# Optimization experiments

Hardware: AMD Instinct MI355X
Metric: run time of the kernel (lower is better)

## Reference

```python
import jax, jax.numpy as jnp
import numpy as np

D_MODEL = 512
N_HEADS = 8
D_HEAD = 64
D_FF = 1024
EPS = 1e-5


def setup_inputs() -> dict:
    key = jax.random.key(0)
    ks = jax.random.split(key, 9)
    B, L = 4, 2048
    s = lambda fan_in: 1.0 / np.sqrt(fan_in)
    return {
        "x": jax.random.normal(ks[0], (B, L, D_MODEL), dtype=jnp.float32),
        "ln1_w": jnp.ones((D_MODEL,), jnp.float32),
        "ln1_b": jnp.zeros((D_MODEL,), jnp.float32),
        "ln2_w": jnp.ones((D_MODEL,), jnp.float32),
        "ln2_b": jnp.zeros((D_MODEL,), jnp.float32),
        "wq": jax.random.normal(ks[1], (D_MODEL, N_HEADS * D_HEAD), jnp.float32) * s(D_MODEL),
        "wk": jax.random.normal(ks[2], (D_MODEL, N_HEADS * D_HEAD), jnp.float32) * s(D_MODEL),
        "wv": jax.random.normal(ks[3], (D_MODEL, N_HEADS * D_HEAD), jnp.float32) * s(D_MODEL),
        "wo": jax.random.normal(ks[4], (N_HEADS * D_HEAD, D_MODEL), jnp.float32) * s(N_HEADS * D_HEAD),
        "w_gate": jax.random.normal(ks[5], (D_MODEL, D_FF), jnp.float32) * s(D_MODEL),
        "w_up": jax.random.normal(ks[6], (D_MODEL, D_FF), jnp.float32) * s(D_MODEL),
        "w_down": jax.random.normal(ks[7], (D_FF, D_MODEL), jnp.float32) * s(D_FF),
    }


def _layernorm(x, w, b):
    mu = jnp.mean(x, axis=-1, keepdims=True)
    var = jnp.var(x, axis=-1, keepdims=True)
    return (x - mu) * jax.lax.rsqrt(var + EPS) * w + b


def reference(x, ln1_w, ln1_b, ln2_w, ln2_b, wq, wk, wv, wo, w_gate, w_up, w_down):
    B, L, _ = x.shape
    scale = D_HEAD ** -0.5

    # --- attention sublayer (pre-LN residual) ---
    h = _layernorm(x, ln1_w, ln1_b)
    q = (h @ wq).reshape(B, L, N_HEADS, D_HEAD)  # [B,L,H,Dh]
    k = (h @ wk).reshape(B, L, N_HEADS, D_HEAD)
    v = (h @ wv).reshape(B, L, N_HEADS, D_HEAD)
    scores = jnp.einsum("bqhd,bkhd->bhqk", q, k) * scale
    # softmax computed in fp32, cast back (matches F.softmax(dtype=float32).to(q.dtype))
    attn = jax.nn.softmax(scores.astype(jnp.float32), axis=-1).astype(q.dtype)
    out = jnp.einsum("bhqk,bkhd->bqhd", attn, v).reshape(B, L, N_HEADS * D_HEAD)
    x = x + out @ wo

    # --- SwiGLU FFN sublayer (pre-LN residual) ---
    h = _layernorm(x, ln2_w, ln2_b)
    gate = jax.nn.silu(h @ w_gate)
    x = x + (gate * (h @ w_up)) @ w_down
    return x
```

## Files before the change

### kernel.cpp

```cpp
#include <hip/hip_runtime.h>
#include <hip/hip_bf16.h>
#include <math.h>

#define EPS 1e-5f

typedef __attribute__((ext_vector_type(8))) short bf16x8;
typedef __attribute__((ext_vector_type(4))) float f32x4;

__device__ __forceinline__ short f2bf(float x) {
    union { float f; unsigned u; } un; un.f = x;
    unsigned r = un.u + 0x7FFF + ((un.u >> 16) & 1);
    return (short)(r >> 16);
}
__device__ __forceinline__ float bf2f(short s) {
    union { unsigned u; float f; } un;
    un.u = ((unsigned)(unsigned short)s) << 16;
    return un.f;
}
__device__ __forceinline__ unsigned pack_bf2(float a, float b) {
    unsigned r;
    asm("v_cvt_pk_bf16_f32 %0, %1, %2" : "=v"(r) : "v"(a), "v"(b));
    return r;
}
__device__ __forceinline__ float exp2_fast(float x) {
    float r;
    asm("v_exp_f32 %0, %1" : "=v"(r) : "v"(x));
    return r;
}
__device__ __forceinline__ void load_lds16(const short* g, short* l) {
    __builtin_amdgcn_global_load_lds(
        (const __attribute__((address_space(1))) unsigned int*)g,
        (__attribute__((address_space(3))) unsigned int*)l, 16, 0, 0);
}

__global__ __launch_bounds__(256) void ln_kernel_b(const float* __restrict__ in,
                                                   const float* __restrict__ w,
                                                   const float* __restrict__ bb,
                                                   short* __restrict__ out) {
    int row = blockIdx.x;
    const float* x = in + (size_t)row * 512;
    short* o = out + (size_t)row * 512;
    int t = threadIdx.x;
    float v0 = x[t], v1 = x[t + 256];
    float s = v0 + v1;
    float s2 = v0 * v0 + v1 * v1;
    for (int off = 32; off > 0; off >>= 1) {
        s  += __shfl_down(s, off);
        s2 += __shfl_down(s2, off);
    }
    __shared__ float rs_[4], rs2_[4];
    __shared__ float mu_s, rstd_s;
    int wid = t >> 6;
    if ((t & 63) == 0) { rs_[wid] = s; rs2_[wid] = s2; }
    __syncthreads();
    if (t == 0) {
        float ts  = rs_[0] + rs_[1] + rs_[2] + rs_[3];
        float ts2 = rs2_[0] + rs2_[1] + rs2_[2] + rs2_[3];
        float mu  = ts * (1.f / 512.f);
        float var = ts2 * (1.f / 512.f) - mu * mu;
        mu_s = mu;
        rstd_s = rsqrtf(var + EPS);
    }
    __syncthreads();
    float mu = mu_s, rstd = rstd_s;
    o[t]       = f2bf((v0 - mu) * rstd * w[t]       + bb[t]);
    o[t + 256] = f2bf((v1 - mu) * rstd * w[t + 256] + bb[t + 256]);
}

struct WT { const float* w; short* t; int K; int N; };
struct WT7 { WT a[7]; };
__global__ __launch_bounds__(256) void transp_w_kernel(WT7 p) {
    WT e = p.a[blockIdx.z];
    int k0 = blockIdx.x * 32, n0 = blockIdx.y * 32;
    if (k0 >= e.K || n0 >= e.N) return;
    __shared__ short t[32][33];
    int tx = threadIdx.x & 31, ty = threadIdx.x >> 5;
#pragma unroll
    for (int pp = 0; pp < 4; pp++)
        t[pp * 8 + ty][tx] = f2bf(e.w[(size_t)(k0 + pp * 8 + ty) * e.N + n0 + tx]);
    __syncthreads();
#pragma unroll
    for (int pp = 0; pp < 4; pp++)
        e.t[(size_t)(n0 + pp * 8 + ty) * e.K + k0 + tx] = t[tx][pp * 8 + ty];
}

template <int EPI>
__global__ __launch_bounds__(256) void gemm_mfma(const short* __restrict__ A,
                                                 const short* __restrict__ Bt,
                                                 const float* __restrict__ res,
                                                 void* __restrict__ Cv,
                                                 int M, int N, int K) {
    __shared__ short As[128 * 64];
    __shared__ short Bs[128 * 64];
    const int tid = threadIdx.x;
    const int lane = tid & 63, w = tid >> 6;
    const int g = lane >> 4, r16 = lane & 15;
    const int wr = w >> 1, wc = w & 1;

    const int nb = gridDim.x * gridDim.y;
    const int fid = blockIdx.y * gridDim.x + blockIdx.x;
    const int nid = (fid & 7) * (nb >> 3) + (fid >> 3);
    const int m0 = (nid / gridDim.x) * 128, n0 = (nid % gridDim.x) * 128;

    const int lr = lane >> 3;
    const int ck = (lane & 7) ^ lr;
    const int row0 = w * 32;

    f32x4 acc[4][4] = {};

    for (int k0 = 0; k0 < K; k0 += 64) {
        __syncthreads();
#pragma unroll
        for (int p = 0; p < 4; p++) {
            int rb = row0 + p * 8;
            load_lds16(&A [(size_t)(m0 + rb + lr) * K + k0 + ck * 8], &As[rb * 64]);
            load_lds16(&Bt[(size_t)(n0 + rb + lr) * K + k0 + ck * 8], &Bs[rb * 64]);
        }
        __syncthreads();
#pragma unroll
        for (int ks = 0; ks < 2; ks++) {
            bf16x8 av[4], bv[4];
#pragma unroll
            for (int i = 0; i < 4; i++) {
                int row = wr * 64 + i * 16 + r16;
                av[i] = *(const bf16x8*)&As[row * 64 + ((ks * 4 + g) ^ (row & 7)) * 8];
            }
#pragma unroll
            for (int j = 0; j < 4; j++) {
                int row = wc * 64 + j * 16 + r16;
                bv[j] = *(const bf16x8*)&Bs[row * 64 + ((ks * 4 + g) ^ (row & 7)) * 8];
            }
#pragma unroll
            for (int i = 0; i < 4; i++)
#pragma unroll
                for (int j = 0; j < 4; j++)
                    acc[i][j] = __builtin_amdgcn_mfma_f32_16x16x32_bf16(av[i], bv[j], acc[i][j], 0, 0, 0);
        }
    }

#pragma unroll
    for (int i = 0; i < 4; i++)
#pragma unroll
        for (int j = 0; j < 4; j++)
#pragma unroll
            for (int jr = 0; jr < 4; jr++) {
                int m = m0 + wr * 64 + i * 16 + 4 * g + jr;
                int n = n0 + wc * 64 + j * 16 + r16;
                float v = acc[i][j][jr];
                if (EPI == 0) {
                    size_t idx = (size_t)m * N + n;
                    ((float*)Cv)[idx] = res[idx] + v;
                } else if (EPI == 2) {
                    if (n < 512) v *= 0.18033688011112042f;
                    ((short*)Cv)[(size_t)(n >> 9) * 4194304 +
                                 (((size_t)(m >> 11) * 8 + ((n >> 6) & 7)) * 2048 + (m & 2047)) * 64 + (n & 63)] = f2bf(v);
                } else {
                    ((short*)Cv)[(size_t)(n >> 10) * 8388608 + (size_t)m * 1024 + (n & 1023)] = f2bf(v);
                }
            }
}

__global__ __launch_bounds__(256) void transp_v_kernel(const short* __restrict__ vb,
                                                       short* __restrict__ vt) {
    __shared__ short tile[64][65];
    int l0 = blockIdx.x * 64;
    int bh = blockIdx.y;
    const size_t base = (size_t)bh * 2048 * 64;
    int tid = threadIdx.x;
#pragma unroll
    for (int p = 0; p < 4; p++) {
        int r = p * 16 + (tid >> 4);
        int c4 = (tid & 15) * 4;
        *(short4*)&tile[r][c4] = *(const short4*)&vb[base + (size_t)(l0 + r) * 64 + c4];
    }
    __syncthreads();
#pragma unroll
    for (int p = 0; p < 4; p++) {
        int d = p * 16 + (tid >> 4);
        int c4 = (tid & 15) * 4;
        short4 o;
        o.x = tile[c4 + 0][d]; o.y = tile[c4 + 1][d];
        o.z = tile[c4 + 2][d]; o.w = tile[c4 + 3][d];
        *(short4*)&vt[base + (size_t)d * 2048 + l0 + c4] = o;
    }
}

__global__ __launch_bounds__(256) void attn_mfma_kernel(const short* __restrict__ qb,
                                                        const short* __restrict__ kb,
                                                        const short* __restrict__ vt,
                                                        short* __restrict__ outb) {
    __shared__ short QP[4096];
    __shared__ short Ks[2][4096];
    __shared__ short Vs[2][4096];

    const int fid = blockIdx.y * 32 + blockIdx.x;
    const int nid = (fid & 7) * 128 + (fid >> 3);
    const int bh = nid >> 5, qt = nid & 31;
    const int b = bh >> 3, h = bh & 7;
    const int q0 = qt * 64;
    const size_t hb = (size_t)bh * (2048 * 64);

    const int tid = threadIdx.x;
    const int lane = tid & 63, w = tid >> 6;
    const int g = lane >> 4, r16 = lane & 15;
    const int lr = lane >> 3, ck = (lane & 7) ^ lr;
    const int rx = r16 & 7;

    load_lds16(&qb[hb + (size_t)(q0 + 16 * w + lr) * 64 + ck * 8], &QP[(16 * w) * 64]);
    load_lds16(&qb[hb + (size_t)(q0 + 16 * w + 8 + lr) * 64 + ck * 8], &QP[(16 * w + 8) * 64]);

    auto stageKV = [&](int buf, int kt) {
        int k0 = kt * 64;
        int rb = w * 16;
        load_lds16(&kb[hb + (size_t)(k0 + rb + lr) * 64 + ck * 8],      &Ks[buf][rb * 64]);
        load_lds16(&kb[hb + (size_t)(k0 + rb + 8 + lr) * 64 + ck * 8],  &Ks[buf][(rb + 8) * 64]);
        load_lds16(&vt[hb + (size_t)(rb + lr) * 2048 + k0 + ck * 8],     &Vs[buf][rb * 64]);
        load_lds16(&vt[hb + (size_t)(rb + 8 + lr) * 2048 + k0 + ck * 8], &Vs[buf][(rb + 8) * 64]);
    };
    stageKV(0, 0);

    bf16x8 aq0, aq1;
    float m_ = -1e30f, l_ = 0.f;
    f32x4 ot[4] = {};
    int cur = 0;

    for (int t = 0; t < 32; t++) {
        __syncthreads();
        if (t == 0) {
            int row = 16 * w + r16;
            aq0 = *(const bf16x8*)&QP[row * 64 + ((0 + g) ^ rx) * 8];
            aq1 = *(const bf16x8*)&QP[row * 64 + ((4 + g) ^ rx) * 8];
        }
        if (t + 1 < 32) stageKV(cur ^ 1, t + 1);
        const short* Kc = &Ks[cur][0];
        const short* Vc = &Vs[cur][0];

        f32x4 s[4];
#pragma unroll
        for (int c = 0; c < 4; c++) {
            int row = 16 * c + r16;
            bf16x8 ak0 = *(const bf16x8*)&Kc[row * 64 + ((0 + g) ^ rx) * 8];
            bf16x8 ak1 = *(const bf16x8*)&Kc[row * 64 + ((4 + g) ^ rx) * 8];
            f32x4 acc = {};
            acc = __builtin_amdgcn_mfma_f32_16x16x32_bf16(ak0, aq0, acc, 0, 0, 0);
            acc = __builtin_amdgcn_mfma_f32_16x16x32_bf16(ak1, aq1, acc, 0, 0, 0);
            s[c] = acc;
        }

        float pmax = s[0][0];
#pragma unroll
        for (int c = 0; c < 4; c++)
#pragma unroll
            for (int jr = 0; jr < 4; jr++)
                if (c || jr) pmax = fmaxf(pmax, s[c][jr]);
        pmax = fmaxf(pmax, __shfl_xor(pmax, 16));
        pmax = fmaxf(pmax, __shfl_xor(pmax, 32));
        if (!__all(pmax - m_ <= 8.f)) {
            float mn = fmaxf(m_, pmax);
            float al = exp2_fast(m_ - mn);
            l_ *= al;
#pragma unroll
            for (int c = 0; c < 4; c++) ot[c] *= al;
            m_ = mn;
        }
        float rs = 0.f;
#pragma unroll
        for (int c = 0; c < 4; c++) {
            float p0 = exp2_fast(s[c][0] - m_);
            float p1 = exp2_fast(s[c][1] - m_);
            float p2 = exp2_fast(s[c][2] - m_);
            float p3 = exp2_fast(s[c][3] - m_);
            rs += (p0 + p1) + (p2 + p3);
            unsigned lo = pack_bf2(p0, p1);
            unsigned hi = pack_bf2(p2, p3);
            int colbase = 16 * c + 4 * g;
            int si = (16 * w + r16) * 64 + (((colbase >> 3) ^ rx) * 8) + (colbase & 7);
            *(unsigned*)&QP[si] = lo;
            *(unsigned*)&QP[si + 2] = hi;
        }
        rs += __shfl_xor(rs, 16);
        rs += __shfl_xor(rs, 32);
        l_ += rs;

        int prow = 16 * w + r16;
        bf16x8 bp0 = *(const bf16x8*)&QP[prow * 64 + ((0 + g) ^ rx) * 8];
        bf16x8 bp1 = *(const bf16x8*)&QP[prow * 64 + ((4 + g) ^ rx) * 8];
#pragma unroll
        for (int c = 0; c < 4; c++) {
            int row = 16 * c + r16;
            bf16x8 av0 = *(const bf16x8*)&Vc[row * 64 + ((0 + g) ^ rx) * 8];
            bf16x8 av1 = *(const bf16x8*)&Vc[row * 64 + ((4 + g) ^ rx) * 8];
            ot[c] = __builtin_amdgcn_mfma_f32_16x16x32_bf16(av0, bp0, ot[c], 0, 0, 0);
            ot[c] = __builtin_amdgcn_mfma_f32_16x16x32_bf16(av1, bp1, ot[c], 0, 0, 0);
        }
        cur ^= 1;
    }

    float inv = 1.f / l_;
    int q = q0 + 16 * w + r16;
#pragma unroll
    for (int c = 0; c < 4; c++) {
        unsigned lo = pack_bf2(ot[c][0] * inv, ot[c][1] * inv);
        unsigned hi = pack_bf2(ot[c][2] * inv, ot[c][3] * inv);
        int d = 16 * c + 4 * g;
        size_t oi = ((size_t)b * 2048 + q) * 512 + h * 64 + d;
        *(unsigned*)&outb[oi] = lo;
        *(unsigned*)&outb[oi + 2] = hi;
    }
}

__global__ __launch_bounds__(256) void silumul_b_kernel(const short* __restrict__ g,
                                                        const short* __restrict__ u,
                                                        short* __restrict__ o) {
    size_t i = ((size_t)blockIdx.x * 256 + threadIdx.x) * 8;
    bf16x8 gv = *(const bf16x8*)&g[i];
    bf16x8 uv = *(const bf16x8*)&u[i];
    bf16x8 ov;
#pragma unroll
    for (int j = 0; j < 8; j++) {
        float x = bf2f(gv[j]);
        float y = x / (1.f + __expf(-x)) * bf2f(uv[j]);
        ov[j] = f2bf(y);
    }
    *(bf16x8*)&o[i] = ov;
}

extern "C" void kernel_launch(void* const* d_in, const int* in_sizes, int n_in,
                              void* d_out, int out_size, void* d_ws, size_t ws_size,
                              hipStream_t stream) {
    const float* x      = (const float*)d_in[0];
    const float* ln1_w  = (const float*)d_in[1];
    const float* ln1_b  = (const float*)d_in[2];
    const float* ln2_w  = (const float*)d_in[3];
    const float* ln2_b  = (const float*)d_in[4];
    const float* wq     = (const float*)d_in[5];
    const float* wk     = (const float*)d_in[6];
    const float* wv     = (const float*)d_in[7];
    const float* wo     = (const float*)d_in[8];
    const float* w_gate = (const float*)d_in[9];
    const float* w_up   = (const float*)d_in[10];
    const float* w_down = (const float*)d_in[11];
    float* out = (float*)d_out;

    const int M = 4 * 2048;
    char* ws = (char*)d_ws;
    const size_t MB = 1 << 20;
    short* h1b   = (short*)(ws);
    short* qb    = (short*)(ws + 8 * MB);
    short* kb    = (short*)(ws + 16 * MB);
    short* vb    = (short*)(ws + 24 * MB);
    short* vt    = (short*)(ws + 32 * MB);
    short* aob   = (short*)(ws + 40 * MB);
    short* g_b   = (short*)(ws + 48 * MB);
    short* u_b   = (short*)(ws + 64 * MB);
    short* qkvT  = (short*)(ws + 80 * MB);
    short* woT   = (short*)(ws + 82 * MB);
    short* wguT  = (short*)(ws + 83 * MB);
    short* wdT   = (short*)(ws + 85 * MB);
    short* h2b   = qb;

    WT7 wt;
    wt.a[0] = {wq,     qkvT,               512,  512};
    wt.a[1] = {wk,     qkvT + 512 * 512,   512,  512};
    wt.a[2] = {wv,     qkvT + 1024 * 512,  512,  512};
    wt.a[3] = {wo,     woT,                512,  512};
    wt.a[4] = {w_gate, wguT,               512, 1024};
    wt.a[5] = {w_up,   wguT + 1024 * 512,  512, 1024};
    wt.a[6] = {w_down, wdT,               1024,  512};

    transp_w_kernel<<<dim3(32, 32, 7), 256, 0, stream>>>(wt);
    ln_kernel_b<<<M, 256, 0, stream>>>(x, ln1_w, ln1_b, h1b);
    gemm_mfma<2><<<dim3(12, 64), 256, 0, stream>>>(h1b, qkvT, nullptr, qb, M, 1536, 512);
    transp_v_kernel<<<dim3(32, 32), 256, 0, stream>>>(vb, vt);
    attn_mfma_kernel<<<dim3(32, 32), 256, 0, stream>>>(qb, kb, vt, aob);
    gemm_mfma<0><<<dim3(4, 64), 256, 0, stream>>>(aob, woT, x, out, M, 512, 512);
    ln_kernel_b<<<M, 256, 0, stream>>>(out, ln2_w, ln2_b, h2b);
    gemm_mfma<3><<<dim3(16, 64), 256, 0, stream>>>(h2b, wguT, nullptr, g_b, M, 2048, 512);
    silumul_b_kernel<<<(M * 1024 / 8 + 255) / 256, 256, 0, stream>>>(g_b, u_b, g_b);
    gemm_mfma<0><<<dim3(4, 64), 256, 0, stream>>>(g_b, wdT, out, out, M, 512, 1024);
}
```

Baseline: 192.1 us.

## Widen attention query tile, fuse SiLU-mul into up GEMM, vectorize layernorm

Three changes. The attention kernel now handles 128 queries per block (two 16-row groups per wave), so each staged K/V tile is reused for twice as many queries and the grid is halved. The gate/up GEMM is split in two, and the up GEMM's epilogue reads the gate output and applies SiLU times up directly, which removes the separate elementwise kernel. LayerNorm now runs one row per wave with float4 loads and a shuffle-only reduction, with no shared memory or block barriers. The trade-offs are higher register pressure in attention, fewer attention blocks for occupancy, and an extra gate-tensor read in the GEMM epilogue.

Result: faster. 183.1 us (-4.7%).

```diff
diff --git a/kernel.cpp b/kernel.cpp
--- a/kernel.cpp
+++ b/kernel.cpp
@@ -37,34 +37,31 @@
                                                    const float* __restrict__ w,
                                                    const float* __restrict__ bb,
                                                    short* __restrict__ out) {
-    int row = blockIdx.x;
-    const float* x = in + (size_t)row * 512;
-    short* o = out + (size_t)row * 512;
-    int t = threadIdx.x;
-    float v0 = x[t], v1 = x[t + 256];
-    float s = v0 + v1;
-    float s2 = v0 * v0 + v1 * v1;
-    for (int off = 32; off > 0; off >>= 1) {
-        s  += __shfl_down(s, off);
-        s2 += __shfl_down(s2, off);
-    }
-    __shared__ float rs_[4], rs2_[4];
-    __shared__ float mu_s, rstd_s;
-    int wid = t >> 6;
-    if ((t & 63) == 0) { rs_[wid] = s; rs2_[wid] = s2; }
-    __syncthreads();
-    if (t == 0) {
-        float ts  = rs_[0] + rs_[1] + rs_[2] + rs_[3];
-        float ts2 = rs2_[0] + rs2_[1] + rs2_[2] + rs2_[3];
-        float mu  = ts * (1.f / 512.f);
-        float var = ts2 * (1.f / 512.f) - mu * mu;
-        mu_s = mu;
-        rstd_s = rsqrtf(var + EPS);
-    }
-    __syncthreads();
-    float mu = mu_s, rstd = rstd_s;
-    o[t]       = f2bf((v0 - mu) * rstd * w[t]       + bb[t]);
-    o[t + 256] = f2bf((v1 - mu) * rstd * w[t + 256] + bb[t + 256]);
+    int wv = threadIdx.x >> 6, lane = threadIdx.x & 63;
+    int row = blockIdx.x * 4 + wv;
+    const float* x = in + (size_t)row * 512 + lane * 8;
+    float4 v0 = *(const float4*)x;
+    float4 v1 = *(const float4*)(x + 4);
+    float s  = (v0.x + v0.y) + (v0.z + v0.w) + (v1.x + v1.y) + (v1.z + v1.w);
+    float s2 = v0.x*v0.x + v0.y*v0.y + v0.z*v0.z + v0.w*v0.w
+             + v1.x*v1.x + v1.y*v1.y + v1.z*v1.z + v1.w*v1.w;
+#pragma unroll
+    for (int off = 1; off < 64; off <<= 1) {
+        s  += __shfl_xor(s, off);
+        s2 += __shfl_xor(s2, off);
+    }
+    float mu = s * (1.f / 512.f);
+    float rstd = rsqrtf(s2 * (1.f / 512.f) - mu * mu + EPS);
+    const float4 wa = *(const float4*)&w[lane * 8];
+    const float4 wb = *(const float4*)&w[lane * 8 + 4];
+    const float4 ba = *(const float4*)&bb[lane * 8];
+    const float4 bv = *(const float4*)&bb[lane * 8 + 4];
+    uint4 o;
+    o.x = pack_bf2((v0.x - mu) * rstd * wa.x + ba.x, (v0.y - mu) * rstd * wa.y + ba.y);
+    o.y = pack_bf2((v0.z - mu) * rstd * wa.z + ba.z, (v0.w - mu) * rstd * wa.w + ba.w);
+    o.z = pack_bf2((v1.x - mu) * rstd * wb.x + bv.x, (v1.y - mu) * rstd * wb.y + bv.y);
+    o.w = pack_bf2((v1.z - mu) * rstd * wb.z + bv.z, (v1.w - mu) * rstd * wb.w + bv.w);
+    *(uint4*)&out[(size_t)row * 512 + lane * 8] = o;
 }
 
 struct WT { const float* w; short* t; int K; int N; };
@@ -88,6 +85,7 @@
 __global__ __launch_bounds__(256) void gemm_mfma(const short* __restrict__ A,
                                                  const short* __restrict__ Bt,
                                                  const float* __restrict__ res,
+                                                 const short* __restrict__ resb,
                                                  void* __restrict__ Cv,
                                                  int M, int N, int K) {
     __shared__ short As[128 * 64];
@@ -150,12 +148,16 @@
                 if (EPI == 0) {
                     size_t idx = (size_t)m * N + n;
                     ((float*)Cv)[idx] = res[idx] + v;
+                } else if (EPI == 1) {
+                    ((short*)Cv)[(size_t)m * N + n] = f2bf(v);
                 } else if (EPI == 2) {
                     if (n < 512) v *= 0.18033688011112042f;
                     ((short*)Cv)[(size_t)(n >> 9) * 4194304 +
                                  (((size_t)(m >> 11) * 8 + ((n >> 6) & 7)) * 2048 + (m & 2047)) * 64 + (n & 63)] = f2bf(v);
                 } else {
-                    ((short*)Cv)[(size_t)(n >> 10) * 8388608 + (size_t)m * 1024 + (n & 1023)] = f2bf(v);
+                    float gt = bf2f(resb[(size_t)m * N + n]);
+                    float y = gt / (1.f + __expf(-gt)) * v;
+                    ((short*)Cv)[(size_t)m * N + n] = f2bf(y);
                 }
             }
 }
@@ -189,15 +191,15 @@
                                                         const short* __restrict__ kb,
                                                         const short* __restrict__ vt,
                                                         short* __restrict__ outb) {
-    __shared__ short QP[4096];
+    __shared__ short QP[128 * 64];
     __shared__ short Ks[2][4096];
     __shared__ short Vs[2][4096];
 
-    const int fid = blockIdx.y * 32 + blockIdx.x;
-    const int nid = (fid & 7) * 128 + (fid >> 3);
-    const int bh = nid >> 5, qt = nid & 31;
+    const int fid = blockIdx.y * gridDim.x + blockIdx.x;
+    const int nid = (fid & 7) * 64 + (fid >> 3);
+    const int bh = nid >> 4, qt = nid & 15;
     const int b = bh >> 3, h = bh & 7;
-    const int q0 = qt * 64;
+    const int q0 = qt * 128;
     const size_t hb = (size_t)bh * (2048 * 64);
 
     const int tid = threadIdx.x;
@@ -206,8 +208,10 @@
     const int lr = lane >> 3, ck = (lane & 7) ^ lr;
     const int rx = r16 & 7;
 
-    load_lds16(&qb[hb + (size_t)(q0 + 16 * w + lr) * 64 + ck * 8], &QP[(16 * w) * 64]);
-    load_lds16(&qb[hb + (size_t)(q0 + 16 * w + 8 + lr) * 64 + ck * 8], &QP[(16 * w + 8) * 64]);
+#pragma unroll
+    for (int p = 0; p < 4; p++)
+        load_lds16(&qb[hb + (size_t)(q0 + 32 * w + 8 * p + lr) * 64 + ck * 8],
+                   &QP[(32 * w + 8 * p) * 64]);
 
     auto stageKV = [&](int buf, int kt) {
         int k0 = kt * 64;
@@ -219,110 +223,119 @@
     };
     stageKV(0, 0);
 
-    bf16x8 aq0, aq1;
-    float m_ = -1e30f, l_ = 0.f;
-    f32x4 ot[4] = {};
+    bf16x8 aqA0, aqA1, aqB0, aqB1;
+    float mA = -1e30f, lA = 0.f, mB = -1e30f, lB = 0.f;
+    f32x4 oA[4] = {}, oB[4] = {};
     int cur = 0;
 
     for (int t = 0; t < 32; t++) {
         __syncthreads();
         if (t == 0) {
-            int row = 16 * w + r16;
-            aq0 = *(const bf16x8*)&QP[row * 64 + ((0 + g) ^ rx) * 8];
-            aq1 = *(const bf16x8*)&QP[row * 64 + ((4 + g) ^ rx) * 8];
+            int rowA = 32 * w + r16, rowB = rowA + 16;
+            aqA0 = *(const bf16x8*)&QP[rowA * 64 + ((0 + g) ^ rx) * 8];
+            aqA1 = *(const bf16x8*)&QP[rowA * 64 + ((4 + g) ^ rx) * 8];
+            aqB0 = *(const bf16x8*)&QP[rowB * 64 + ((0 + g) ^ rx) * 8];
+            aqB1 = *(const bf16x8*)&QP[rowB * 64 + ((4 + g) ^ rx) * 8];
         }
         if (t + 1 < 32) stageKV(cur ^ 1, t + 1);
         const short* Kc = &Ks[cur][0];
         const short* Vc = &Vs[cur][0];
 
-        f32x4 s[4];
+        f32x4 sA[4], sB[4];
 #pragma unroll
         for (int c = 0; c < 4; c++) {
             int row = 16 * c + r16;
             bf16x8 ak0 = *(const bf16x8*)&Kc[row * 64 + ((0 + g) ^ rx) * 8];
             bf16x8 ak1 = *(const bf16x8*)&Kc[row * 64 + ((4 + g) ^ rx) * 8];
-            f32x4 acc = {};
-            acc = __builtin_amdgcn_mfma_f32_16x16x32_bf16(ak0, aq0, acc, 0, 0, 0);
-            acc = __builtin_amdgcn_mfma_f32_16x16x32_bf16(ak1, aq1, acc, 0, 0, 0);
-            s[c] = acc;
-        }
-
-        float pmax = s[0][0];
+            f32x4 a1 = {}, a2 = {};
+            a1 = __builtin_amdgcn_mfma_f32_16x16x32_bf16(ak0, aqA0, a1, 0, 0, 0);
+            a1 = __builtin_amdgcn_mfma_f32_16x16x32_bf16(ak1, aqA1, a1, 0, 0, 0);
+            a2 = __builtin_amdgcn_mfma_f32_16x16x32_bf16(ak0, aqB0, a2, 0, 0, 0);
+            a2 = __builtin_amdgcn_mfma_f32_16x16x32_bf16(ak1, aqB1, a2, 0, 0, 0);
+            sA[c] = a1; sB[c] = a2;
+        }
+
+        float pmA = sA[0][0], pmB = sB[0][0];
 #pragma unroll
         for (int c = 0; c < 4; c++)
 #pragma unroll
-            for (int jr = 0; jr < 4; jr++)
-                if (c || jr) pmax = fmaxf(pmax, s[c][jr]);
-        pmax = fmaxf(pmax, __shfl_xor(pmax, 16));
-        pmax = fmaxf(pmax, __shfl_xor(pmax, 32));
-        if (!__all(pmax - m_ <= 8.f)) {
-            float mn = fmaxf(m_, pmax);
-            float al = exp2_fast(m_ - mn);
-            l_ *= al;
-#pragma unroll
-            for (int c = 0; c < 4; c++) ot[c] *= al;
-            m_ = mn;
-        }
-        float rs = 0.f;
+            for (int jr = 0; jr < 4; jr++) {
+                if (c || jr) {
+                    pmA = fmaxf(pmA, sA[c][jr]);
+                    pmB = fmaxf(pmB, sB[c][jr]);
+                }
+            }
+        pmA = fmaxf(pmA, __shfl_xor(pmA, 16));
+        pmA = fmaxf(pmA, __shfl_xor(pmA, 32));
+        pmB = fmaxf(pmB, __shfl_xor(pmB, 16));
+        pmB = fmaxf(pmB, __shfl_xor(pmB, 32));
+        if (!__all((pmA - mA <= 8.f) && (pmB - mB <= 8.f))) {
+            float mnA = fmaxf(mA, pmA), mnB = fmaxf(mB, pmB);
+            float alA = exp2_fast(mA - mnA), alB = exp2_fast(mB - mnB);
+            lA *= alA; lB *= alB;
+#pragma unroll
+            for (int c = 0; c < 4; c++) { oA[c] *= alA; oB[c] *= alB; }
+            mA = mnA; mB = mnB;
+        }
+        float rsA = 0.f, rsB = 0.f;
+        int prA = 32 * w + r16, prB = prA + 16;
 #pragma unroll
         for (int c = 0; c < 4; c++) {
-            float p0 = exp2_fast(s[c][0] - m_);
-            float p1 = exp2_fast(s[c][1] - m_);
-            float p2 = exp2_fast(s[c][2] - m_);
-            float p3 = exp2_fast(s[c][3] - m_);
-            rs += (p0 + p1) + (p2 + p3);
-            unsigned lo = pack_bf2(p0, p1);
-            unsigned hi = pack_bf2(p2, p3);
             int colbase = 16 * c + 4 * g;
-            int si = (16 * w + r16) * 64 + (((colbase >> 3) ^ rx) * 8) + (colbase & 7);
-            *(unsigned*)&QP[si] = lo;
-            *(unsigned*)&QP[si + 2] = hi;
-        }
-        rs += __shfl_xor(rs, 16);
-        rs += __shfl_xor(rs, 32);
-        l_ += rs;
-
-        int prow = 16 * w + r16;
-        bf16x8 bp0 = *(const bf16x8*)&QP[prow * 64 + ((0 + g) ^ rx) * 8];
-        bf16x8 bp1 = *(const bf16x8*)&QP[prow * 64 + ((4 + g) ^ rx) * 8];
+            int co = (((colbase >> 3) ^ rx) * 8) + (colbase & 7);
+            {
+                float p0 = exp2_fast(sA[c][0] - mA), p1 = exp2_fast(sA[c][1] - mA);
+                float p2 = exp2_fast(sA[c][2] - mA), p3 = exp2_fast(sA[c][3] - mA);
+                rsA += (p0 + p1) + (p2 + p3);
+                unsigned long long pv = (unsigned long long)pack_bf2(p0, p1)
+                                      | ((unsigned long long)pack_bf2(p2, p3) << 32);
+                *(unsigned long long*)&QP[prA * 64 + co] = pv;
+            }
+            {
+                float p0 = exp2_fast(sB[c][0] - mB), p1 = exp2_fast(sB[c][1] - mB);
+                float p2 = exp2_fast(sB[c][2] - mB), p3 = exp2_fast(sB[c][3] - mB);
+                rsB += (p0 + p1) + (p2 + p3);
+                unsigned long long pv = (unsigned long long)pack_bf2(p0, p1)
+                                      | ((unsigned long long)pack_bf2(p2, p3) << 32);
+                *(unsigned long long*)&QP[prB * 64 + co] = pv;
+            }
+        }
+        rsA += __shfl_xor(rsA, 16); rsA += __shfl_xor(rsA, 32); lA += rsA;
+        rsB += __shfl_xor(rsB, 16); rsB += __shfl_xor(rsB, 32); lB += rsB;
+
+        bf16x8 bpA0 = *(const bf16x8*)&QP[prA * 64 + ((0 + g) ^ rx) * 8];
+        bf16x8 bpA1 = *(const bf16x8*)&QP[prA * 64 + ((4 + g) ^ rx) * 8];
+        bf16x8 bpB0 = *(const bf16x8*)&QP[prB * 64 + ((0 + g) ^ rx) * 8];
+        bf16x8 bpB1 = *(const bf16x8*)&QP[prB * 64 + ((4 + g) ^ rx) * 8];
 #pragma unroll
         for (int c = 0; c < 4; c++) {
             int row = 16 * c + r16;
             bf16x8 av0 = *(const bf16x8*)&Vc[row * 64 + ((0 + g) ^ rx) * 8];
             bf16x8 av1 = *(const bf16x8*)&Vc[row * 64 + ((4 + g) ^ rx) * 8];
-            ot[c] = __builtin_amdgcn_mfma_f32_16x16x32_bf16(av0, bp0, ot[c], 0, 0, 0);
-            ot[c] = __builtin_amdgcn_mfma_f32_16x16x32_bf16(av1, bp1, ot[c], 0, 0, 0);
+            oA[c] = __builtin_amdgcn_mfma_f32_16x16x32_bf16(av0, bpA0, oA[c], 0, 0, 0);
+            oA[c] = __builtin_amdgcn_mfma_f32_16x16x32_bf16(av1, bpA1, oA[c], 0, 0, 0);
+            oB[c] = __builtin_amdgcn_mfma_f32_16x16x32_bf16(av0, bpB0, oB[c], 0, 0, 0);
+            oB[c] = __builtin_amdgcn_mfma_f32_16x16x32_bf16(av1, bpB1, oB[c], 0, 0, 0);
         }
         cur ^= 1;
     }
 
-    float inv = 1.f / l_;
-    int q = q0 + 16 * w + r16;
+    float ivA = 1.f / lA, ivB = 1.f / lB;
+    int qa = q0 + 32 * w + r16;
 #pragma unroll
     for (int c = 0; c < 4; c++) {
-        unsigned lo = pack_bf2(ot[c][0] * inv, ot[c][1] * inv);
-        unsigned hi = pack_bf2(ot[c][2] * inv, ot[c][3] * inv);
         int d = 16 * c + 4 * g;
-        size_t oi = ((size_t)b * 2048 + q) * 512 + h * 64 + d;
-        *(unsigned*)&outb[oi] = lo;
-        *(unsigned*)&outb[oi + 2] = hi;
-    }
-}
-
-__global__ __launch_bounds__(256) void silumul_b_kernel(const short* __restrict__ g,
-                                                        const short* __restrict__ u,
-                                                        short* __restrict__ o) {
-    size_t i = ((size_t)blockIdx.x * 256 + threadIdx.x) * 8;
-    bf16x8 gv = *(const bf16x8*)&g[i];
-    bf16x8 uv = *(const bf16x8*)&u[i];
-    bf16x8 ov;
-#pragma unroll
-    for (int j = 0; j < 8; j++) {
-        float x = bf2f(gv[j]);
-        float y = x / (1.f + __expf(-x)) * bf2f(uv[j]);
-        ov[j] = f2bf(y);
-    }
-    *(bf16x8*)&o[i] = ov;
+        {
+            unsigned long long pv = (unsigned long long)pack_bf2(oA[c][0] * ivA, oA[c][1] * ivA)
+                                  | ((unsigned long long)pack_bf2(oA[c][2] * ivA, oA[c][3] * ivA) << 32);
+            *(unsigned long long*)&outb[((size_t)b * 2048 + qa) * 512 + h * 64 + d] = pv;
+        }
+        {
+            unsigned long long pv = (unsigned long long)pack_bf2(oB[c][0] * ivB, oB[c][1] * ivB)
+                                  | ((unsigned long long)pack_bf2(oB[c][2] * ivB, oB[c][3] * ivB) << 32);
+            *(unsigned long long*)&outb[((size_t)b * 2048 + qa + 16) * 512 + h * 64 + d] = pv;
+        }
+    }
 }
 
 extern "C" void kernel_launch(void* const* d_in, const int* in_sizes, int n_in,
@@ -369,13 +382,13 @@
     wt.a[6] = {w_down, wdT,               1024,  512};
 
     transp_w_kernel<<<dim3(32, 32, 7), 256, 0, stream>>>(wt);
-    ln_kernel_b<<<M, 256, 0, stream>>>(x, ln1_w, ln1_b, h1b);
-    gemm_mfma<2><<<dim3(12, 64), 256, 0, stream>>>(h1b, qkvT, nullptr, qb, M, 1536, 512);
+    ln_kernel_b<<<M / 4, 256, 0, stream>>>(x, ln1_w, ln1_b, h1b);
+    gemm_mfma<2><<<dim3(12, 64), 256, 0, stream>>>(h1b, qkvT, nullptr, nullptr, qb, M, 1536, 512);
     transp_v_kernel<<<dim3(32, 32), 256, 0, stream>>>(vb, vt);
-    attn_mfma_kernel<<<dim3(32, 32), 256, 0, stream>>>(qb, kb, vt, aob);
-    gemm_mfma<0><<<dim3(4, 64), 256, 0, stream>>>(aob, woT, x, out, M, 512, 512);
-    ln_kernel_b<<<M, 256, 0, stream>>>(out, ln2_w, ln2_b, h2b);
-    gemm_mfma<3><<<dim3(16, 64), 256, 0, stream>>>(h2b, wguT, nullptr, g_b, M, 2048, 512);
-    silumul_b_kernel<<<(M * 1024 / 8 + 255) / 256, 256, 0, stream>>>(g_b, u_b, g_b);
-    gemm_mfma<0><<<dim3(4, 64), 256, 0, stream>>>(g_b, wdT, out, out, M, 512, 1024);
-}
+    attn_mfma_kernel<<<dim3(16, 32), 256, 0, stream>>>(qb, kb, vt, aob);
+    gemm_mfma<0><<<dim3(4, 64), 256, 0, stream>>>(aob, woT, x, nullptr, out, M, 512, 512);
+    ln_kernel_b<<<M / 4, 256, 0, stream>>>(out, ln2_w, ln2_b, h2b);
+    gemm_mfma<1><<<dim3(8, 64), 256, 0, stream>>>(h2b, wguT, nullptr, nullptr, g_b, M, 1024, 512);
+    gemm_mfma<4><<<dim3(8, 64), 256, 0, stream>>>(h2b, wguT + 1024 * 512, nullptr, g_b, u_b, M, 1024, 512);
+    gemm_mfma<0><<<dim3(4, 64), 256, 0, stream>>>(u_b, wdT, out, nullptr, out, M, 512, 1024);
+}
```
